# Optimization experiments

Hardware: AMD Instinct MI355X
Metric: run time of the kernel (lower is better)

## Reference

```python
import jax, jax.numpy as jnp
import numpy as np

IN_FEATURES = 2048
HIDDEN_DIM = 1024
ENC_DIM = 1024
DEC_DIM = IN_FEATURES - ENC_DIM
MASK_VAL = -50000.0


def setup_inputs() -> dict:
    key = jax.random.key(0)
    k1, k2, k3, k4, k5 = jax.random.split(key, 5)
    B, S = 32, 2048
    encoder_outputs = jax.random.normal(k1, (B, S, ENC_DIM), dtype=jnp.float32)
    decoder_state = jax.random.normal(k2, (B, DEC_DIM), dtype=jnp.float32)
    # lengths in [1, S]
    sequence_length = jax.random.randint(k3, (B,), 1, S + 1).astype(jnp.int64)
    # fc_w: Linear(in_features, hidden_dim, bias=False) -> weight [hidden, in_feat]
    W = jax.random.normal(k4, (HIDDEN_DIM, IN_FEATURES), dtype=jnp.float32) / np.sqrt(IN_FEATURES)
    # fc_v: Linear(hidden_dim, 1, bias=False) -> weight [1, hidden]; store as [hidden]
    v = jax.random.normal(k5, (HIDDEN_DIM,), dtype=jnp.float32) / np.sqrt(HIDDEN_DIM)
    return {"encoder_outputs": encoder_outputs, "sequence_length": sequence_length,
            "decoder_state": decoder_state, "W": W, "v": v}


def reference(encoder_outputs, sequence_length, decoder_state, W, v):
    # score = v^T tanh(W [h; s]) == v^T tanh(W_enc h + W_dec s)  (avoids concat)
    W_enc = W[:, :ENC_DIM]      # [H, De]
    W_dec = W[:, ENC_DIM:]      # [H, Dd]
    # [B, S, H] + [B, 1, H]
    hidden = jnp.tanh(jnp.einsum('bse,he->bsh', encoder_outputs, W_enc)
                      + jnp.einsum('bd,hd->bh', decoder_state, W_dec)[:, None, :])
    logits = jnp.einsum('bsh,h->bs', hidden, v)                      # [B, S]
    S = logits.shape[1]
    mask = jnp.arange(S)[None, :] < sequence_length[:, None]          # [B, S]
    masked_logits = jnp.where(mask, logits, jnp.float32(MASK_VAL))
    attn_weight = jax.nn.softmax(masked_logits, axis=1)               # [B, S]
    out = jnp.einsum('bs,bse->be', attn_weight, encoder_outputs)      # [B, De]
    return (out, attn_weight)
```

## Files before the change

### kernel.cpp

```cpp
#include <hip/hip_runtime.h>
#include <hip/hip_bf16.h>

#define B 32
#define S 2048
#define E 1024
#define H 1024
#define MASK_VAL -50000.0f

typedef __attribute__((ext_vector_type(8))) short bf16x8_t;
typedef __attribute__((ext_vector_type(4))) float f32x4_t;

__device__ __forceinline__ float fast_tanh(float x) {
    float a = fabsf(x);
    float e = __expf(-2.0f * a);
    float t = (1.0f - e) / (1.0f + e);
    return copysignf(t, x);
}

__device__ __forceinline__ float b2f(short s) {
    return __uint_as_float(((unsigned)(unsigned short)s) << 16);
}

__device__ __forceinline__ bf16x8_t cvt8(const float4 f0, const float4 f1) {
    union { bf16x8_t s8; __hip_bfloat162 h[4]; } u;
    u.h[0] = __float22bfloat162_rn(make_float2(f0.x, f0.y));
    u.h[1] = __float22bfloat162_rn(make_float2(f0.z, f0.w));
    u.h[2] = __float22bfloat162_rn(make_float2(f1.x, f1.y));
    u.h[3] = __float22bfloat162_rn(make_float2(f1.z, f1.w));
    return u.s8;
}

__device__ __forceinline__ void gload16(const void* g, void* l) {
    __builtin_amdgcn_global_load_lds(
        (const __attribute__((address_space(1))) void*)g,
        (__attribute__((address_space(3))) void*)l, 16, 0, 0);
}

__global__ __launch_bounds__(256) void kprep(
    const float* __restrict__ W, const float* __restrict__ dec,
    __hip_bfloat16* __restrict__ Wb, float* __restrict__ dec_proj)
{
    int blk = blockIdx.x, tid = threadIdx.x;
    if (blk < 1024) {
        int idx = (blk * 256 + tid) * 4;
        int h = idx >> 10, e = idx & 1023;
        float4 f = *(const float4*)(W + (size_t)h * 2048 + e);
        __hip_bfloat162 p0 = __float22bfloat162_rn(make_float2(f.x, f.y));
        __hip_bfloat162 p1 = __float22bfloat162_rn(make_float2(f.z, f.w));
        *reinterpret_cast<__hip_bfloat162*>(Wb + idx)     = p0;
        *reinterpret_cast<__hip_bfloat162*>(Wb + idx + 2) = p1;
    } else {
        int h = blk - 1024;
        __shared__ float4 wlds[256];
        wlds[tid] = *(const float4*)(W + (size_t)h * 2048 + 1024 + tid * 4);
        __syncthreads();
        int b = tid >> 3, chunk = tid & 7;
        const float4* dd = (const float4*)(dec + b * 1024 + chunk * 128);
        float acc = 0.f;
        #pragma unroll
        for (int i = 0; i < 32; ++i) {
            float4 w4 = wlds[chunk * 32 + i];
            float4 d4 = dd[i];
            acc += w4.x * d4.x + w4.y * d4.y + w4.z * d4.z + w4.w * d4.w;
        }
        acc += __shfl_xor(acc, 1);
        acc += __shfl_xor(acc, 2);
        acc += __shfl_xor(acc, 4);
        if (chunk == 0) dec_proj[b * H + h] = acc;
    }
}

template<int MODE>
__global__ __launch_bounds__(256, 2) void k2_mfma(
    const float* __restrict__ enc, __hip_bfloat16* __restrict__ encb,
    const __hip_bfloat16* __restrict__ Wb, const float* __restrict__ v,
    const float* __restrict__ dec_proj, const int* __restrict__ seq,
    float* __restrict__ part)
{
    const int bid = blockIdx.x;
    int pair, ht;
    if (MODE == 1) {
        pair = bid; ht = 0;
    } else if (MODE == 0) {
        const int xcd = bid & 7, j = bid >> 3;
        pair = (j / 7) * 8 + xcd; ht = j % 7 + 1;
    } else {
        pair = (bid >> 6) * 8 + (bid & 7); ht = (bid >> 3) & 7;
    }
    const int b  = pair >> 4;
    const int s0 = (pair & 15) * 128;
    if (s0 >= seq[b]) return;
    const int h0 = ht * 128;

    const int tid  = threadIdx.x;
    const int wave = tid >> 6;
    const int lane = tid & 63;
    const int wr = wave >> 1, wc = wave & 1;
    const int cr = lane & 15, cg = lane >> 4;

    __shared__ __hip_bfloat16 Al[2][128 * 64];
    __shared__ __hip_bfloat16 Bl[2][128 * 64];

    const int colb  = (tid & 7) * 16;
    const int rbase = tid >> 3;

    f32x4_t acc[4][4];
    #pragma unroll
    for (int m = 0; m < 4; ++m)
        #pragma unroll
        for (int n = 0; n < 4; ++n)
            acc[m][n] = (f32x4_t){0.f, 0.f, 0.f, 0.f};

    auto stage = [&](int buf, int kt) {
        #pragma unroll
        for (int i = 0; i < 4; ++i) {
            const int row   = i * 32 + rbase;
            const int scolb = colb ^ ((row & 7) << 4);
            const __hip_bfloat16* bg =
                Wb + (((size_t)(h0 + row)) << 10) + kt * 64 + (scolb >> 1);
            gload16(bg, (char*)&Bl[buf][0] + (i * 256 + tid) * 16);
            if (MODE == 0) {
                const __hip_bfloat16* ag =
                    encb + (((size_t)b * S + s0 + row) << 10) + kt * 64 + (scolb >> 1);
                gload16(ag, (char*)&Al[buf][0] + (i * 256 + tid) * 16);
            } else {
                const size_t aoff = (((size_t)b * S + s0 + row) << 10)
                                  + kt * 64 + (tid & 7) * 8;
                const float* af = enc + aoff;
                bf16x8_t v8 = cvt8(*(const float4*)af, *(const float4*)(af + 4));
                *(bf16x8_t*)((char*)&Al[buf][0] + row * 128 + scolb) = v8;
                if (MODE == 1)
                    *(bf16x8_t*)(encb + aoff) = v8;
            }
        }
    };

    stage(0, 0);
    __syncthreads();
    int cur = 0;
    for (int kt = 0; kt < 16; ++kt) {
        if (kt < 15) stage(cur ^ 1, kt + 1);
        bf16x8_t afr[2][4], bfr[2][4];
        #pragma unroll
        for (int ks = 0; ks < 2; ++ks) {
            #pragma unroll
            for (int m = 0; m < 4; ++m) {
                const int arow  = wr * 64 + m * 16 + cr;
                const int acolb = (ks * 64 + cg * 16) ^ ((arow & 7) << 4);
                afr[ks][m] = *(const bf16x8_t*)((const char*)&Al[cur][0] + arow * 128 + acolb);
                const int brow  = wc * 64 + m * 16 + cr;
                const int bcolb = (ks * 64 + cg * 16) ^ ((brow & 7) << 4);
                bfr[ks][m] = *(const bf16x8_t*)((const char*)&Bl[cur][0] + brow * 128 + bcolb);
            }
        }
        #pragma unroll
        for (int ks = 0; ks < 2; ++ks)
            #pragma unroll
            for (int m = 0; m < 4; ++m)
                #pragma unroll
                for (int n = 0; n < 4; ++n)
                    acc[m][n] = __builtin_amdgcn_mfma_f32_16x16x32_bf16(
                        afr[ks][m], bfr[ks][n], acc[m][n], 0, 0, 0);
        __syncthreads();
        cur ^= 1;
    }

    float vv[4], dp[4];
    #pragma unroll
    for (int n = 0; n < 4; ++n) {
        int h = h0 + wc * 64 + n * 16 + cr;
        vv[n] = v[h];
        dp[n] = dec_proj[b * H + h];
    }
    #pragma unroll
    for (int m = 0; m < 4; ++m) {
        #pragma unroll
        for (int j = 0; j < 4; ++j) {
            float t = 0.f;
            #pragma unroll
            for (int n = 0; n < 4; ++n)
                t += vv[n] * fast_tanh(acc[m][n][j] + dp[n]);
            t += __shfl_xor(t, 1);
            t += __shfl_xor(t, 2);
            t += __shfl_xor(t, 4);
            t += __shfl_xor(t, 8);
            if (cr == 0) {
                int srow = s0 + wr * 64 + m * 16 + cg * 4 + j;
                part[(size_t)(b * S + srow) * 16 + ht * 2 + wc] = t;
            }
        }
    }
}

__global__ __launch_bounds__(256) void k3_softmax(
    const float* __restrict__ part, const int* __restrict__ seq,
    float* __restrict__ attn)
{
    int b = blockIdx.x, tid = threadIdx.x;
    int len = seq[b];
    float vals[8];
    float mx = -3.4e38f;
    #pragma unroll
    for (int i = 0; i < 8; ++i) {
        int s = i * 256 + tid;
        float x = MASK_VAL;
        if (s < len) {
            const f32x4_t* p = (const f32x4_t*)&part[(size_t)(b * S + s) * 16];
            f32x4_t a = p[0], c = p[1], d = p[2], e = p[3];
            x = (a[0] + a[1] + a[2] + a[3]) + (c[0] + c[1] + c[2] + c[3]) +
                (d[0] + d[1] + d[2] + d[3]) + (e[0] + e[1] + e[2] + e[3]);
        }
        vals[i] = x;
        mx = fmaxf(mx, x);
    }
    #pragma unroll
    for (int off = 1; off < 64; off <<= 1) mx = fmaxf(mx, __shfl_xor(mx, off));
    __shared__ float red[8];
    int wave = tid >> 6, lane = tid & 63;
    if (lane == 0) red[wave] = mx;
    __syncthreads();
    mx = fmaxf(fmaxf(red[0], red[1]), fmaxf(red[2], red[3]));
    float e[8];
    float sum = 0.f;
    #pragma unroll
    for (int i = 0; i < 8; ++i) { e[i] = __expf(vals[i] - mx); sum += e[i]; }
    #pragma unroll
    for (int off = 1; off < 64; off <<= 1) sum += __shfl_xor(sum, off);
    if (lane == 0) red[4 + wave] = sum;
    __syncthreads();
    sum = red[4] + red[5] + red[6] + red[7];
    float inv = 1.0f / sum;
    #pragma unroll
    for (int i = 0; i < 8; ++i) attn[b * S + i * 256 + tid] = e[i] * inv;
}

template<int AMODE>
__global__ __launch_bounds__(256) void k4_partial(
    const float* __restrict__ enc, const __hip_bfloat16* __restrict__ encb,
    const float* __restrict__ attn, const int* __restrict__ seq,
    float* __restrict__ opart)
{
    int c = blockIdx.x, b = blockIdx.y, tid = threadIdx.x;
    int base_s = c * 128;
    int len = seq[b];
    if (AMODE == 0) {
        int e0 = (tid & 127) * 8;
        int so = tid >> 7;
        float av[8];
        #pragma unroll
        for (int j = 0; j < 8; ++j) av[j] = 0.f;
        if (base_s < len) {
            int s_end = min(128, len - base_s);
            for (int s = so; s < s_end; s += 2) {
                float w = attn[b * S + base_s + s];
                bf16x8_t u = *(const bf16x8_t*)(encb +
                    (((size_t)b * S + base_s + s) << 10) + e0);
                #pragma unroll
                for (int j = 0; j < 8; ++j) av[j] += w * b2f(u[j]);
            }
        }
        float* dst = opart + (((size_t)(b * 16 + c) * 2 + so) << 10) + e0;
        *(float4*)dst       = make_float4(av[0], av[1], av[2], av[3]);
        *(float4*)(dst + 4) = make_float4(av[4], av[5], av[6], av[7]);
    } else {
        float4 acc = make_float4(0.f, 0.f, 0.f, 0.f);
        if (base_s < len) {
            int s_end = min(128, len - base_s);
            const float* ep = enc + (((size_t)b * S + base_s) << 10) + tid * 4;
            const float* ap = attn + b * S + base_s;
            for (int s = 0; s < s_end; ++s) {
                float w = ap[s];
                float4 ev = *(const float4*)ep;
                ep += E;
                acc.x += w * ev.x; acc.y += w * ev.y;
                acc.z += w * ev.z; acc.w += w * ev.w;
            }
        }
        float* dst = opart + (((size_t)(b * 16 + c) * 2) << 10) + tid * 4;
        *(float4*)dst = acc;
        float* dst2 = opart + (((size_t)(b * 16 + c) * 2 + 1) << 10) + tid * 4;
        *(float4*)dst2 = make_float4(0.f, 0.f, 0.f, 0.f);
    }
}

__global__ __launch_bounds__(256) void k5_reduce(
    const float* __restrict__ opart, float* __restrict__ out)
{
    int gid = blockIdx.x * 256 + threadIdx.x;
    int b = gid >> 10, e = gid & 1023;
    float s = 0.f;
    #pragma unroll
    for (int c = 0; c < 32; ++c) s += opart[((size_t)(b * 32 + c) << 10) + e];
    out[gid] = s;
}

extern "C" void kernel_launch(void* const* d_in, const int* in_sizes, int n_in,
                              void* d_out, int out_size, void* d_ws, size_t ws_size,
                              hipStream_t stream)
{
    const float* enc = (const float*)d_in[0];
    const int*   seq = (const int*)d_in[1];
    const float* dec = (const float*)d_in[2];
    const float* W   = (const float*)d_in[3];
    const float* v   = (const float*)d_in[4];

    float* out  = (float*)d_out;
    float* attn = out + B * E;

    float* dec_proj = (float*)d_ws;
    float* part     = dec_proj + B * H;
    float* opart    = part + (size_t)B * S * 16;
    __hip_bfloat16* Wb = (__hip_bfloat16*)(opart + (size_t)B * 32 * 1024);
    __hip_bfloat16* encb = Wb + (size_t)H * E;

    const size_t need = (size_t)(B * H + B * S * 16 + B * 32 * 1024) * 4
                      + (size_t)H * E * 2 + (size_t)B * S * E * 2;
    const bool use_encb = ws_size >= need;

    hipLaunchKernelGGL(kprep, dim3(2048), dim3(256), 0, stream,
                       W, dec, Wb, dec_proj);
    if (use_encb) {
        hipLaunchKernelGGL(k2_mfma<1>, dim3(512), dim3(256), 0, stream,
                           enc, encb, Wb, v, dec_proj, seq, part);
        hipLaunchKernelGGL(k2_mfma<0>, dim3(3584), dim3(256), 0, stream,
                           enc, encb, Wb, v, dec_proj, seq, part);
    } else {
        hipLaunchKernelGGL(k2_mfma<2>, dim3(4096), dim3(256), 0, stream,
                           enc, encb, Wb, v, dec_proj, seq, part);
    }
    hipLaunchKernelGGL(k3_softmax, dim3(B), dim3(256), 0, stream,
                       part, seq, attn);
    if (use_encb) {
        hipLaunchKernelGGL(k4_partial<0>, dim3(16, B), dim3(256), 0, stream,
                           enc, encb, attn, seq, opart);
    } else {
        hipLaunchKernelGGL(k4_partial<1>, dim3(16, B), dim3(256), 0, stream,
                           enc, encb, attn, seq, opart);
    }
    hipLaunchKernelGGL(k5_reduce, dim3(B * E / 256), dim3(256), 0, stream,
                       opart, out);
}
```

Measured before the change: 245.6 us.

## Move fp32-to-bf16 encoder conversion into prep kernel and unify GEMM grid

Before, the first head tile of the score GEMM (MODE 1) converted encoder outputs to bf16 while also computing, and seven more head tiles followed in a second launch. Now a standalone conversion branch in the fused prep kernel writes encb, skipping rows past each sequence length, and the bf16 GEMM runs all eight head tiles in one launch of 4096 blocks. This removes a kernel launch and the tail imbalance between the two GEMM launches. In exchange, encoder data is read once more to do the conversion with no overlapped compute. The tanh division is also replaced by a hardware reciprocal.

```diff
diff --git a/kernel.cpp b/kernel.cpp
--- a/kernel.cpp
+++ b/kernel.cpp
@@ -13,7 +13,7 @@
 __device__ __forceinline__ float fast_tanh(float x) {
     float a = fabsf(x);
     float e = __expf(-2.0f * a);
-    float t = (1.0f - e) / (1.0f + e);
+    float t = (1.0f - e) * __builtin_amdgcn_rcpf(1.0f + e);
     return copysignf(t, x);
 }
 
@@ -36,9 +36,11 @@
         (__attribute__((address_space(3))) void*)l, 16, 0, 0);
 }
 
-__global__ __launch_bounds__(256) void kprep(
+__global__ __launch_bounds__(256) void kfused0(
     const float* __restrict__ W, const float* __restrict__ dec,
-    __hip_bfloat16* __restrict__ Wb, float* __restrict__ dec_proj)
+    const float* __restrict__ enc, const int* __restrict__ seq,
+    __hip_bfloat16* __restrict__ Wb, float* __restrict__ dec_proj,
+    __hip_bfloat16* __restrict__ encb)
 {
     int blk = blockIdx.x, tid = threadIdx.x;
     if (blk < 1024) {
@@ -49,7 +51,7 @@
         __hip_bfloat162 p1 = __float22bfloat162_rn(make_float2(f.z, f.w));
         *reinterpret_cast<__hip_bfloat162*>(Wb + idx)     = p0;
         *reinterpret_cast<__hip_bfloat162*>(Wb + idx + 2) = p1;
-    } else {
+    } else if (blk < 2048) {
         int h = blk - 1024;
         __shared__ float4 wlds[256];
         wlds[tid] = *(const float4*)(W + (size_t)h * 2048 + 1024 + tid * 4);
@@ -67,28 +69,35 @@
         acc += __shfl_xor(acc, 2);
         acc += __shfl_xor(acc, 4);
         if (chunk == 0) dec_proj[b * H + h] = acc;
+    } else {
+        int g = blk - 2048;
+        int c = g & 15, b = g >> 4;
+        if (c * 128 >= seq[b]) return;
+        size_t base = ((size_t)b * S + c * 128) << 10;
+        const float* src = enc + base;
+        __hip_bfloat16* dst = encb + base;
+        #pragma unroll 4
+        for (int it = 0; it < 64; ++it) {
+            int idx = it * 2048 + tid * 8;
+            float4 f0 = *(const float4*)(src + idx);
+            float4 f1 = *(const float4*)(src + idx + 4);
+            *(bf16x8_t*)(dst + idx) = cvt8(f0, f1);
+        }
     }
 }
 
 template<int MODE>
 __global__ __launch_bounds__(256, 2) void k2_mfma(
-    const float* __restrict__ enc, __hip_bfloat16* __restrict__ encb,
+    const float* __restrict__ enc, const __hip_bfloat16* __restrict__ encb,
     const __hip_bfloat16* __restrict__ Wb, const float* __restrict__ v,
     const float* __restrict__ dec_proj, const int* __restrict__ seq,
     float* __restrict__ part)
 {
-    const int bid = blockIdx.x;
-    int pair, ht;
-    if (MODE == 1) {
-        pair = bid; ht = 0;
-    } else if (MODE == 0) {
-        const int xcd = bid & 7, j = bid >> 3;
-        pair = (j / 7) * 8 + xcd; ht = j % 7 + 1;
-    } else {
-        pair = (bid >> 6) * 8 + (bid & 7); ht = (bid >> 3) & 7;
-    }
-    const int b  = pair >> 4;
-    const int s0 = (pair & 15) * 128;
+    const int bid  = blockIdx.x;
+    const int pair = (bid >> 6) * 8 + (bid & 7);
+    const int ht   = (bid >> 3) & 7;
+    const int b    = pair >> 4;
+    const int s0   = (pair & 15) * 128;
     if (s0 >= seq[b]) return;
     const int h0 = ht * 128;
 
@@ -124,13 +133,10 @@
                     encb + (((size_t)b * S + s0 + row) << 10) + kt * 64 + (scolb >> 1);
                 gload16(ag, (char*)&Al[buf][0] + (i * 256 + tid) * 16);
             } else {
-                const size_t aoff = (((size_t)b * S + s0 + row) << 10)
-                                  + kt * 64 + (tid & 7) * 8;
-                const float* af = enc + aoff;
+                const float* af =
+                    enc + (((size_t)b * S + s0 + row) << 10) + kt * 64 + (tid & 7) * 8;
                 bf16x8_t v8 = cvt8(*(const float4*)af, *(const float4*)(af + 4));
                 *(bf16x8_t*)((char*)&Al[buf][0] + row * 128 + scolb) = v8;
-                if (MODE == 1)
-                    *(bf16x8_t*)(encb + aoff) = v8;
             }
         }
     };
@@ -317,14 +323,14 @@
                       + (size_t)H * E * 2 + (size_t)B * S * E * 2;
     const bool use_encb = ws_size >= need;
 
-    hipLaunchKernelGGL(kprep, dim3(2048), dim3(256), 0, stream,
-                       W, dec, Wb, dec_proj);
     if (use_encb) {
-        hipLaunchKernelGGL(k2_mfma<1>, dim3(512), dim3(256), 0, stream,
-                           enc, encb, Wb, v, dec_proj, seq, part);
-        hipLaunchKernelGGL(k2_mfma<0>, dim3(3584), dim3(256), 0, stream,
+        hipLaunchKernelGGL(kfused0, dim3(2560), dim3(256), 0, stream,
+                           W, dec, enc, seq, Wb, dec_proj, encb);
+        hipLaunchKernelGGL(k2_mfma<0>, dim3(4096), dim3(256), 0, stream,
                            enc, encb, Wb, v, dec_proj, seq, part);
     } else {
+        hipLaunchKernelGGL(kfused0, dim3(2048), dim3(256), 0, stream,
+                           W, dec, enc, seq, Wb, dec_proj, encb);
         hipLaunchKernelGGL(k2_mfma<2>, dim3(4096), dim3(256), 0, stream,
                            enc, encb, Wb, v, dec_proj, seq, part);
     }
```

After: 223.8 us. -8.9%, faster.
